# Kernel optimization log

Hardware: AMD Instinct MI355X
Metric: run time of the kernel (lower is better)

The kernel has to match this reference:

```python
import jax, jax.numpy as jnp
import numpy as np

DIM = 1024
HEADS = 16
HEAD_DIM = DIM // HEADS
SCALE = HEAD_DIM ** -0.5
HIDDEN = 4 * DIM
EPS = 1e-5


def _ln(x, g, b):
    m = jnp.mean(x, -1, keepdims=True)
    v = jnp.mean(jnp.square(x - m), -1, keepdims=True)
    return (x - m) / jnp.sqrt(v + EPS) * g + b


def _attn(x, wqkv, qb, vb, wp, bp):
    # x: (B, N, C). qkv bias = concat(q_bias, zeros, v_bias) as in the torch code.
    B, N, C = x.shape
    bias = jnp.concatenate([qb, jnp.zeros_like(vb), vb])
    qkv = (x @ wqkv.T + bias).reshape(B, N, 3, HEADS, HEAD_DIM).transpose(2, 0, 3, 1, 4)
    q, k, v = qkv[0], qkv[1], qkv[2]
    # qk_float=True: logits computed in float32
    logits = jnp.einsum('bhqd,bhkd->bhqk', (q * SCALE).astype(jnp.float32), k.astype(jnp.float32))
    a = jax.nn.softmax(logits, axis=-1).astype(x.dtype)
    o = jnp.einsum('bhqk,bhkd->bqhd', a, v).reshape(B, N, C)
    return o @ wp.T + bp


def setup_inputs() -> dict:
    key = jax.random.key(0)
    ks = jax.random.split(key, 16)
    s = 0.02
    d = {
        'x': jax.random.normal(ks[0], (4, 8, 196, DIM), jnp.float32),
        'cls_token': jax.random.normal(ks[1], (4, DIM), jnp.float32),
        # temporal branch
        'tln_g': jnp.ones((DIM,), jnp.float32), 'tln_b': jnp.zeros((DIM,), jnp.float32),
        't_wqkv': jax.random.normal(ks[2], (3 * DIM, DIM), jnp.float32) * s,
        't_qb': jax.random.normal(ks[3], (DIM,), jnp.float32) * s,
        't_vb': jax.random.normal(ks[4], (DIM,), jnp.float32) * s,
        't_wproj': jax.random.normal(ks[5], (DIM, DIM), jnp.float32) * s,
        't_bproj': jnp.zeros((DIM,), jnp.float32),
        't_fc_w': jax.random.normal(ks[6], (DIM, DIM), jnp.float32) * s,
        't_fc_b': jnp.zeros((DIM,), jnp.float32),
        # spatial branch
        'n1_g': jnp.ones((DIM,), jnp.float32), 'n1_b': jnp.zeros((DIM,), jnp.float32),
        's_wqkv': jax.random.normal(ks[7], (3 * DIM, DIM), jnp.float32) * s,
        's_qb': jax.random.normal(ks[8], (DIM,), jnp.float32) * s,
        's_vb': jax.random.normal(ks[9], (DIM,), jnp.float32) * s,
        's_wproj': jax.random.normal(ks[10], (DIM, DIM), jnp.float32) * s,
        's_bproj': jnp.zeros((DIM,), jnp.float32),
        # mlp
        'n2_g': jnp.ones((DIM,), jnp.float32), 'n2_b': jnp.zeros((DIM,), jnp.float32),
        'fc1_w': jax.random.normal(ks[11], (HIDDEN, DIM), jnp.float32) * s,
        'fc1_b': jnp.zeros((HIDDEN,), jnp.float32),
        'fc2_w': jax.random.normal(ks[12], (DIM, HIDDEN), jnp.float32) * s,
        'fc2_b': jnp.zeros((DIM,), jnp.float32),
    }
    return d


def reference(x, cls_token, tln_g, tln_b, t_wqkv, t_qb, t_vb, t_wproj, t_bproj,
              t_fc_w, t_fc_b, n1_g, n1_b, s_wqkv, s_qb, s_vb, s_wproj, s_bproj,
              n2_g, n2_b, fc1_w, fc1_b, fc2_w, fc2_b):
    B, T, N, C = x.shape
    # temporal attention: 'b t n m -> (b n) t m'
    xt = x.transpose(0, 2, 1, 3).reshape(B * N, T, C)
    xt = _attn(_ln(xt, tln_g, tln_b), t_wqkv, t_qb, t_vb, t_wproj, t_bproj)
    # '(b n) t m -> b (n t) m'
    xt = xt.reshape(B, N * T, C)
    xt = xt @ t_fc_w.T + t_fc_b
    xt = x.transpose(0, 2, 1, 3).reshape(B, N * T, C) + xt
    # spatial attention with cls token per frame
    init_cls = cls_token[:, None, :]                               # (B, 1, C)
    cls_rep = jnp.broadcast_to(init_cls, (B, T, C)).reshape(B * T, 1, C)
    xs = xt.reshape(B, N, T, C).transpose(0, 2, 1, 3).reshape(B * T, N, C)
    xs = jnp.concatenate([cls_rep, xs], axis=1)                    # (B*T, N+1, C)
    xs = _attn(_ln(xs, n1_g, n1_b), s_wqkv, s_qb, s_vb, s_wproj, s_bproj)
    cls_m = xs[:, 0, :].reshape(B, T, C).mean(axis=1, keepdims=True)  # (B, 1, C)
    xs = xs[:, 1:, :].reshape(B, T, N, C).transpose(0, 2, 1, 3).reshape(B, N * T, C)
    x2 = jnp.concatenate([init_cls, xt], axis=1) + jnp.concatenate([cls_m, xs], axis=1)
    # MLP (exact GELU, matching nn.GELU default)
    h = _ln(x2, n2_g, n2_b)
    h = jax.nn.gelu(h @ fc1_w.T + fc1_b, approximate=False) @ fc2_w.T + fc2_b
    x2 = x2 + h
    cls_out = x2[:, 0, :]
    xo = x2[:, 1:].reshape(B, N, T, C).transpose(0, 2, 1, 3)       # (B, T, N, C)
    return xo, cls_out
```

## Files before the change

### kernel.cpp

```cpp
#include <hip/hip_runtime.h>
#include <stdint.h>


#define SCALE 0.125f

typedef unsigned short u16;
typedef short bf16x8 __attribute__((ext_vector_type(8)));
typedef float f32x4 __attribute__((ext_vector_type(4)));

static constexpr int kNT    = 1568;
static constexpr int kRowsA = 6272;
static constexpr int kSeqS  = 197;
static constexpr int kRowsS = 6304;
static constexpr int kRowsC = 6276;
static constexpr size_t kXO = 6422528;

__device__ __forceinline__ float bf2f(u16 u) {
    union { unsigned int i; float f; } c; c.i = ((unsigned int)u) << 16; return c.f;
}
__device__ __forceinline__ u16 f2bf(float f) {
    union { float f; unsigned int i; } c; c.f = f;
    unsigned int r = c.i + 0x7FFFu + ((c.i >> 16) & 1u);
    return (u16)(r >> 16);
}

__device__ __forceinline__ void gll16(const void* g, void* l) {
    __builtin_amdgcn_global_load_lds((__attribute__((address_space(1))) void*)g,
                                     (__attribute__((address_space(3))) void*)l,
                                     16, 0, 0);
}

__global__ void convw_k(const float* __restrict__ in, u16* __restrict__ out, int n4) {
    const int stride = gridDim.x * blockDim.x;
    for (int i = blockIdx.x * blockDim.x + threadIdx.x; i < n4; i += stride) {
        float4 v = ((const float4*)in)[i];
        ushort4 o;
        o.x = f2bf(v.x); o.y = f2bf(v.y); o.z = f2bf(v.z); o.w = f2bf(v.w);
        ((ushort4*)out)[i] = o;
    }
}

__global__ void bias3_k(const float* __restrict__ qb, const float* __restrict__ vb,
                        float* __restrict__ dst) {
    const int i = blockIdx.x * 256 + threadIdx.x;
    if (i >= 3072) return;
    dst[i] = (i < 1024) ? qb[i] : (i < 2048) ? 0.0f : vb[i - 2048];
}

template<int MODE>
__global__ void ln_k(const float* __restrict__ src, const float* __restrict__ src2,
                     const float* __restrict__ g, const float* __restrict__ bt,
                     u16* __restrict__ out, int rows) {
    const int r = (blockIdx.x << 2) + (threadIdx.x >> 6);
    const int lane = threadIdx.x & 63;
    if (r >= rows) return;
    const float* srow;
    if constexpr (MODE == 0) {
        int b = r / kNT, rem = r - b * kNT, n = rem >> 3, t = rem & 7;
        srow = src + (((size_t)((b * 8 + t) * 196 + n)) << 10);
    } else if constexpr (MODE == 1) {
        int s2 = r / kSeqS, i = r - s2 * kSeqS, b = s2 >> 3, t = s2 & 7;
        srow = (i == 0) ? (src2 + ((size_t)b << 10))
                        : (src + (((size_t)(b * kNT + ((i - 1) << 3) + t)) << 10));
    } else {
        srow = src + ((size_t)r << 10);
    }
    float4 v[4]; float s = 0.f, ss = 0.f;
#pragma unroll
    for (int j = 0; j < 4; ++j) {
        v[j] = *(const float4*)&srow[((j << 6) + lane) << 2];
        s  += v[j].x + v[j].y + v[j].z + v[j].w;
        ss += v[j].x * v[j].x + v[j].y * v[j].y + v[j].z * v[j].z + v[j].w * v[j].w;
    }
#pragma unroll
    for (int off = 1; off < 64; off <<= 1) { s += __shfl_xor(s, off); ss += __shfl_xor(ss, off); }
    const float mean = s * (1.f / 1024.f);
    const float rstd = rsqrtf(ss * (1.f / 1024.f) - mean * mean + 1e-5f);
#pragma unroll
    for (int j = 0; j < 4; ++j) {
        const int c = ((j << 6) + lane) << 2;
        float4 gg = *(const float4*)&g[c];
        float4 bb = *(const float4*)&bt[c];
        ushort4 o;
        o.x = f2bf((v[j].x - mean) * rstd * gg.x + bb.x);
        o.y = f2bf((v[j].y - mean) * rstd * gg.y + bb.y);
        o.z = f2bf((v[j].z - mean) * rstd * gg.z + bb.z);
        o.w = f2bf((v[j].w - mean) * rstd * gg.w + bb.w);
        *(ushort4*)&out[((size_t)r << 10) + c] = o;
    }
}

template<int MODE>
__global__ void gemm_bt(const u16* __restrict__ A, const u16* __restrict__ W,
                        const float* __restrict__ bias,
                        u16* __restrict__ outB, float* __restrict__ outF,
                        const float* __restrict__ resid, float* __restrict__ dout,
                        int M, int N, int K) {
    __shared__ __align__(16) u16 As[128 * 32];
    __shared__ __align__(16) u16 Bs[128 * 32];
    const int tid  = threadIdx.x;
    const int lane = tid & 63, wave = tid >> 6;
    const int lo = lane & 15, hi = lane >> 4;
    const int wr = wave >> 1, wc = wave & 1;
    const int row0 = blockIdx.y << 7, col0 = blockIdx.x << 7;

    const int c0 = (wave << 7) + lane;
    const int c1 = c0 + 64;
    int ar0 = row0 + (c0 >> 2); if (ar0 > M - 1) ar0 = M - 1;
    int ar1 = row0 + (c1 >> 2); if (ar1 > M - 1) ar1 = M - 1;
    int br0 = col0 + (c0 >> 2); if (br0 > N - 1) br0 = N - 1;
    int br1 = col0 + (c1 >> 2); if (br1 > N - 1) br1 = N - 1;
    const u16* aS0 = A + (size_t)ar0 * K + ((c0 & 3) << 3);
    const u16* aS1 = A + (size_t)ar1 * K + ((c1 & 3) << 3);
    const u16* bS0 = W + (size_t)br0 * K + ((c0 & 3) << 3);
    const u16* bS1 = W + (size_t)br1 * K + ((c1 & 3) << 3);
    u16* lA0 = &As[wave << 10];
    u16* lA1 = &As[(wave << 10) + 512];
    u16* lB0 = &Bs[wave << 10];
    u16* lB1 = &Bs[(wave << 10) + 512];

    f32x4 acc[4][4] = {};

    for (int k0 = 0; k0 < K; k0 += 32) {
        gll16(aS0 + k0, lA0);
        gll16(aS1 + k0, lA1);
        gll16(bS0 + k0, lB0);
        gll16(bS1 + k0, lB1);
        __syncthreads();
        bf16x8 af[4], bfr[4];
#pragma unroll
        for (int m = 0; m < 4; ++m)
            af[m] = *(const bf16x8*)&As[((wr << 6) + (m << 4) + lo) * 32 + (hi << 3)];
#pragma unroll
        for (int n = 0; n < 4; ++n)
            bfr[n] = *(const bf16x8*)&Bs[((wc << 6) + (n << 4) + lo) * 32 + (hi << 3)];
#pragma unroll
        for (int m = 0; m < 4; ++m)
#pragma unroll
            for (int n = 0; n < 4; ++n)
                acc[m][n] = __builtin_amdgcn_mfma_f32_16x16x32_bf16(af[m], bfr[n], acc[m][n], 0, 0, 0);
        __syncthreads();
    }

#pragma unroll
    for (int m = 0; m < 4; ++m) {
        const int rb = row0 + (wr << 6) + (m << 4) + (hi << 2);
#pragma unroll
        for (int n = 0; n < 4; ++n) {
            const int c = col0 + (wc << 6) + (n << 4) + lo;
            const float bc = bias[c];
#pragma unroll
            for (int j = 0; j < 4; ++j) {
                const int r = rb + j;
                if (r >= M) continue;
                float v = acc[m][n][j] + bc;
                if constexpr (MODE == 2) v = 0.5f * v * (1.0f + erff(v * 0.70710678f));
                if constexpr (MODE == 3) {
                    int b = r / 1568, rem = r - b * 1568, nn = rem >> 3, tt = rem & 7;
                    v += resid[(((size_t)((b * 8 + tt) * 196 + nn)) << 10) + c];
                }
                if constexpr (MODE == 0 || MODE == 2) {
                    outB[(size_t)r * N + c] = f2bf(v);
                } else if constexpr (MODE == 1 || MODE == 3) {
                    outF[(size_t)r * N + c] = v;
                } else {
                    v += resid[((size_t)r << 10) + c];
                    int b = r / 1569, i = r - b * 1569;
                    if (i == 0) dout[kXO + ((size_t)b << 10) + c] = v;
                    else {
                        int jj = i - 1, nn = jj >> 3, tt = jj & 7;
                        dout[(((size_t)((b * 8 + tt) * 196 + nn)) << 10) + c] = v;
                    }
                }
            }
        }
    }
}

__global__ void attn_a_k(const u16* __restrict__ qkv, u16* __restrict__ o) {
    __shared__ float lq[4][8][65], lk[4][8][65], lv[4][8][65];
    __shared__ float al[4][64];
    const int lane = threadIdx.x & 63, wave = threadIdx.x >> 6;
    const int p = (blockIdx.x << 2) + wave;
    const int s = p >> 4, h = p & 15;
    const u16* base = qkv + (size_t)s * 24576 + (h << 6);
    for (int u = lane; u < 1536; u += 64) {
        const int part = u >> 9, t = (u >> 6) & 7, d = u & 63;
        const float val = bf2f(base[(size_t)t * 3072 + (part << 10) + d]);
        if (part == 0) lq[wave][t][d] = val;
        else if (part == 1) lk[wave][t][d] = val;
        else lv[wave][t][d] = val;
    }
    __syncthreads();
    const int qi = lane >> 3, kj = lane & 7;
    float dot = 0.f;
#pragma unroll
    for (int d = 0; d < 64; ++d) dot += lq[wave][qi][d] * lk[wave][kj][d];
    dot *= SCALE;
    float m = dot;
    m = fmaxf(m, __shfl_xor(m, 1));
    m = fmaxf(m, __shfl_xor(m, 2));
    m = fmaxf(m, __shfl_xor(m, 4));
    const float e = expf(dot - m);
    float sm = e;
    sm += __shfl_xor(sm, 1);
    sm += __shfl_xor(sm, 2);
    sm += __shfl_xor(sm, 4);
    al[wave][lane] = e / sm;
    __syncthreads();
    u16* orow = o + (size_t)s * 8192 + (h << 6) + lane;
#pragma unroll
    for (int ii = 0; ii < 8; ++ii) {
        float accv = 0.f;
#pragma unroll
        for (int jj = 0; jj < 8; ++jj) accv += al[wave][(ii << 3) + jj] * lv[wave][jj][lane];
        orow[(size_t)ii * 1024] = f2bf(accv);
    }
}

__global__ __launch_bounds__(256, 2) void attn_s_mfma(const u16* __restrict__ qkv,
                                                      u16* __restrict__ o) {
    __shared__ __align__(16) u16 SM[29696];
    u16* __restrict__ Vt = SM;
    const int tid = threadIdx.x, lane = tid & 63, wave = tid >> 6;
    const int lo = lane & 15, hi = lane >> 4;
    u16* __restrict__ Pw = SM + 14848 + wave * 3712;
    const int s2 = blockIdx.x >> 4, h = blockIdx.x & 15;
    const u16* __restrict__ base = qkv + (size_t)s2 * (kSeqS * 3072) + (h << 6);

    for (int u = tid; u < 26 * 64; u += 256) {
        const int d = u & 63, k0 = (u >> 6) << 3;
        union { bf16x8 v; u16 e[8]; } pk;
#pragma unroll
        for (int i = 0; i < 8; ++i) {
            int kr = k0 + i; if (kr > 196) kr = 196;
            pk.e[i] = base[(size_t)kr * 3072 + 2048 + d];
        }
        *(bf16x8*)&Vt[d * 232 + k0] = pk.v;
    }
    for (int u = tid; u < 1024; u += 256)
        Vt[(u >> 4) * 232 + 208 + (u & 15)] = 0;
    for (int u = lane; u < 256; u += 64)
        Pw[(u >> 4) * 232 + 208 + (u & 15)] = 0;
    __syncthreads();

    for (int qt = wave; qt < 13; qt += 4) {
        int qr = qt * 16 + lo; if (qr > 196) qr = 196;
        const u16* qp = base + (size_t)qr * 3072;
        const bf16x8 aq0 = *(const bf16x8*)&qp[hi << 3];
        const bf16x8 aq1 = *(const bf16x8*)&qp[32 + (hi << 3)];

        f32x4 s[13];
#pragma unroll
        for (int kt = 0; kt < 13; ++kt) {
            int kr = kt * 16 + lo; if (kr > 196) kr = 196;
            const u16* kp = base + (size_t)kr * 3072 + 1024;
            const bf16x8 bk0 = *(const bf16x8*)&kp[hi << 3];
            const bf16x8 bk1 = *(const bf16x8*)&kp[32 + (hi << 3)];
            f32x4 acc = {};
            acc = __builtin_amdgcn_mfma_f32_16x16x32_bf16(aq0, bk0, acc, 0, 0, 0);
            acc = __builtin_amdgcn_mfma_f32_16x16x32_bf16(aq1, bk1, acc, 0, 0, 0);
            s[kt] = acc * SCALE;
        }
        if (lo > 4) s[12] = (f32x4){-1e30f, -1e30f, -1e30f, -1e30f};

        float inv[4];
#pragma unroll
        for (int j = 0; j < 4; ++j) {
            float m = s[0][j];
#pragma unroll
            for (int kt = 1; kt < 13; ++kt) m = fmaxf(m, s[kt][j]);
            m = fmaxf(m, __shfl_xor(m, 1));
            m = fmaxf(m, __shfl_xor(m, 2));
            m = fmaxf(m, __shfl_xor(m, 4));
            m = fmaxf(m, __shfl_xor(m, 8));
            float sum = 0.f;
#pragma unroll
            for (int kt = 0; kt < 13; ++kt) {
                const float e = __expf(s[kt][j] - m);
                s[kt][j] = e;
                sum += e;
            }
            sum += __shfl_xor(sum, 1);
            sum += __shfl_xor(sum, 2);
            sum += __shfl_xor(sum, 4);
            sum += __shfl_xor(sum, 8);
            inv[j] = 1.f / sum;
        }

#pragma unroll
        for (int kt = 0; kt < 13; ++kt)
#pragma unroll
            for (int j = 0; j < 4; ++j)
                Pw[((hi << 2) + j) * 232 + kt * 16 + lo] = f2bf(s[kt][j]);

        f32x4 o4[4] = {};
#pragma unroll
        for (int kc = 0; kc < 7; ++kc) {
            const bf16x8 pa = *(const bf16x8*)&Pw[lo * 232 + kc * 32 + (hi << 3)];
#pragma unroll
            for (int dt = 0; dt < 4; ++dt) {
                const bf16x8 vf = *(const bf16x8*)&Vt[(dt * 16 + lo) * 232 + kc * 32 + (hi << 3)];
                o4[dt] = __builtin_amdgcn_mfma_f32_16x16x32_bf16(pa, vf, o4[dt], 0, 0, 0);
            }
        }

#pragma unroll
        for (int j = 0; j < 4; ++j) {
            const int q = qt * 16 + (hi << 2) + j;
            if (q > 196) continue;
            u16* orow = o + (((size_t)(s2 * kSeqS + q)) << 10) + (h << 6);
#pragma unroll
            for (int dt = 0; dt < 4; ++dt)
                orow[dt * 16 + lo] = f2bf(o4[dt][j] * inv[j]);
        }
    }
}

__global__ void clsm_k(const float* __restrict__ xs, float* __restrict__ cm) {
    const int idx = blockIdx.x * 256 + threadIdx.x;
    if (idx >= 4096) return;
    const int b = idx >> 10, c = idx & 1023;
    float s = 0.f;
#pragma unroll
    for (int t = 0; t < 8; ++t) s += xs[(((size_t)(b * 8 + t)) * kSeqS) * 1024 + c];
    cm[idx] = s * 0.125f;
}

__global__ void build_x2_k(const float* __restrict__ xt, const float* __restrict__ xs,
                           const float* __restrict__ cls, const float* __restrict__ cm,
                           float* __restrict__ x2) {
    const int r = blockIdx.x;
    const int c = threadIdx.x << 2;
    const int b = r / 1569, i = r - b * 1569;
    const float* pa; const float* pb;
    if (i == 0) {
        pa = cls + ((size_t)b << 10) + c;
        pb = cm + ((size_t)b << 10) + c;
    } else {
        const int jj = i - 1, n = jj >> 3, t = jj & 7;
        pa = xt + (((size_t)(b * 1568 + jj)) << 10) + c;
        pb = xs + (((size_t)((b * 8 + t) * kSeqS + 1 + n)) << 10) + c;
    }
    const float4 va = *(const float4*)pa;
    const float4 vb = *(const float4*)pb;
    float4 vo;
    vo.x = va.x + vb.x; vo.y = va.y + vb.y; vo.z = va.z + vb.z; vo.w = va.w + vb.w;
    *(float4*)&x2[((size_t)r << 10) + c] = vo;
}

extern "C" void kernel_launch(void* const* d_in, const int* in_sizes, int n_in,
                              void* d_out, int out_size, void* d_ws, size_t ws_size,
                              hipStream_t stream) {
    const float* x       = (const float*)d_in[0];
    const float* cls     = (const float*)d_in[1];
    const float* tln_g   = (const float*)d_in[2];
    const float* tln_b   = (const float*)d_in[3];
    const float* t_wqkv  = (const float*)d_in[4];
    const float* t_qb    = (const float*)d_in[5];
    const float* t_vb    = (const float*)d_in[6];
    const float* t_wproj = (const float*)d_in[7];
    const float* t_bproj = (const float*)d_in[8];
    const float* t_fc_w  = (const float*)d_in[9];
    const float* t_fc_b  = (const float*)d_in[10];
    const float* n1_g    = (const float*)d_in[11];
    const float* n1_b    = (const float*)d_in[12];
    const float* s_wqkv  = (const float*)d_in[13];
    const float* s_qb    = (const float*)d_in[14];
    const float* s_vb    = (const float*)d_in[15];
    const float* s_wproj = (const float*)d_in[16];
    const float* s_bproj = (const float*)d_in[17];
    const float* n2_g    = (const float*)d_in[18];
    const float* n2_b    = (const float*)d_in[19];
    const float* fc1_w   = (const float*)d_in[20];
    const float* fc1_b   = (const float*)d_in[21];
    const float* fc2_w   = (const float*)d_in[22];
    const float* fc2_b   = (const float*)d_in[23];
    float* dout = (float*)d_out;
    char* ws = (char*)d_ws;

    size_t off = 0;
    auto alloc = [&](size_t bytes) { size_t o = off; off += (bytes + 255) & ~(size_t)255; return o; };

    u16* t_wqkv_bf  = (u16*)(ws + alloc(3145728ull * 2));
    u16* t_wproj_bf = (u16*)(ws + alloc(1048576ull * 2));
    u16* t_fcw_bf   = (u16*)(ws + alloc(1048576ull * 2));
    u16* s_wqkv_bf  = (u16*)(ws + alloc(3145728ull * 2));
    u16* s_wproj_bf = (u16*)(ws + alloc(1048576ull * 2));
    u16* fc1_bf     = (u16*)(ws + alloc(4194304ull * 2));
    u16* fc2_bf     = (u16*)(ws + alloc(4194304ull * 2));
    u16* ln_bf      = (u16*)(ws + alloc((size_t)kRowsS * 1024 * 2));
    u16* qkv_bf     = (u16*)(ws + alloc((size_t)kRowsS * 3072 * 2));
    u16* o_bf       = (u16*)(ws + alloc((size_t)kRowsS * 1024 * 2));
    u16* h1_bf      = qkv_bf;
    u16* mid_bf     = (u16*)(ws + alloc((size_t)kRowsA * 1024 * 2));
    float* xt_f     = (float*)(ws + alloc((size_t)kRowsA * 1024 * 4));
    float* xs_f     = (float*)(ws + alloc((size_t)kRowsS * 1024 * 4));
    float* x2_f     = (float*)(ws + alloc((size_t)kRowsC * 1024 * 4));
    float* bias_t   = (float*)(ws + alloc(3072 * 4));
    float* bias_s   = (float*)(ws + alloc(3072 * 4));
    float* clsm     = (float*)(ws + alloc(4096 * 4));
    (void)ws_size; (void)in_sizes; (void)n_in; (void)out_size;

    convw_k<<<dim3(1024), dim3(256), 0, stream>>>(t_wqkv, t_wqkv_bf, 786432);
    convw_k<<<dim3(512),  dim3(256), 0, stream>>>(t_wproj, t_wproj_bf, 262144);
    convw_k<<<dim3(512),  dim3(256), 0, stream>>>(t_fc_w, t_fcw_bf, 262144);
    convw_k<<<dim3(1024), dim3(256), 0, stream>>>(s_wqkv, s_wqkv_bf, 786432);
    convw_k<<<dim3(512),  dim3(256), 0, stream>>>(s_wproj, s_wproj_bf, 262144);
    convw_k<<<dim3(1024), dim3(256), 0, stream>>>(fc1_w, fc1_bf, 1048576);
    convw_k<<<dim3(1024), dim3(256), 0, stream>>>(fc2_w, fc2_bf, 1048576);
    bias3_k<<<dim3(12), dim3(256), 0, stream>>>(t_qb, t_vb, bias_t);
    bias3_k<<<dim3(12), dim3(256), 0, stream>>>(s_qb, s_vb, bias_s);

    ln_k<0><<<dim3(kRowsA / 4), dim3(256), 0, stream>>>(x, nullptr, tln_g, tln_b, ln_bf, kRowsA);
    gemm_bt<0><<<dim3(24, 49), dim3(256), 0, stream>>>(ln_bf, t_wqkv_bf, bias_t, qkv_bf, nullptr, nullptr, nullptr, kRowsA, 3072, 1024);
    attn_a_k<<<dim3(3136), dim3(256), 0, stream>>>(qkv_bf, o_bf);
    gemm_bt<0><<<dim3(8, 49), dim3(256), 0, stream>>>(o_bf, t_wproj_bf, t_bproj, mid_bf, nullptr, nullptr, nullptr, kRowsA, 1024, 1024);
    gemm_bt<3><<<dim3(8, 49), dim3(256), 0, stream>>>(mid_bf, t_fcw_bf, t_fc_b, nullptr, xt_f, x, nullptr, kRowsA, 1024, 1024);

    ln_k<1><<<dim3(kRowsS / 4), dim3(256), 0, stream>>>(xt_f, cls, n1_g, n1_b, ln_bf, kRowsS);
    gemm_bt<0><<<dim3(24, 50), dim3(256), 0, stream>>>(ln_bf, s_wqkv_bf, bias_s, qkv_bf, nullptr, nullptr, nullptr, kRowsS, 3072, 1024);
    attn_s_mfma<<<dim3(512), dim3(256), 0, stream>>>(qkv_bf, o_bf);
    gemm_bt<1><<<dim3(8, 50), dim3(256), 0, stream>>>(o_bf, s_wproj_bf, s_bproj, nullptr, xs_f, nullptr, nullptr, kRowsS, 1024, 1024);
    clsm_k<<<dim3(16), dim3(256), 0, stream>>>(xs_f, clsm);
    build_x2_k<<<dim3(kRowsC), dim3(256), 0, stream>>>(xt_f, xs_f, cls, clsm, x2_f);

    ln_k<2><<<dim3(kRowsC / 4), dim3(256), 0, stream>>>(x2_f, nullptr, n2_g, n2_b, ln_bf, kRowsC);
    gemm_bt<2><<<dim3(32, 50), dim3(256), 0, stream>>>(ln_bf, fc1_bf, fc1_b, h1_bf, nullptr, nullptr, nullptr, kRowsC, 4096, 1024);
    gemm_bt<4><<<dim3(8, 50), dim3(256), 0, stream>>>(h1_bf, fc2_bf, fc2_b, nullptr, nullptr, x2_f, dout, kRowsC, 1024, 4096);
}
```

Baseline: 550.9 us.

## Double-buffer GEMM LDS tiles with K=64 steps and XOR-swizzled layout

```diff
diff --git a/kernel.cpp b/kernel.cpp
--- a/kernel.cpp
+++ b/kernel.cpp
@@ -91,55 +91,83 @@
 }
 
 template<int MODE>
-__global__ void gemm_bt(const u16* __restrict__ A, const u16* __restrict__ W,
-                        const float* __restrict__ bias,
-                        u16* __restrict__ outB, float* __restrict__ outF,
-                        const float* __restrict__ resid, float* __restrict__ dout,
-                        int M, int N, int K) {
-    __shared__ __align__(16) u16 As[128 * 32];
-    __shared__ __align__(16) u16 Bs[128 * 32];
+__global__ __launch_bounds__(256, 2) void gemm_bt(
+        const u16* __restrict__ A, const u16* __restrict__ W,
+        const float* __restrict__ bias,
+        u16* __restrict__ outB, float* __restrict__ outF,
+        const float* __restrict__ resid, float* __restrict__ dout,
+        int M, int N, int K) {
+    __shared__ __align__(16) u16 As[2][8192];
+    __shared__ __align__(16) u16 Bs[2][8192];
     const int tid  = threadIdx.x;
     const int lane = tid & 63, wave = tid >> 6;
     const int lo = lane & 15, hi = lane >> 4;
     const int wr = wave >> 1, wc = wave & 1;
     const int row0 = blockIdx.y << 7, col0 = blockIdx.x << 7;
 
-    const int c0 = (wave << 7) + lane;
-    const int c1 = c0 + 64;
-    int ar0 = row0 + (c0 >> 2); if (ar0 > M - 1) ar0 = M - 1;
-    int ar1 = row0 + (c1 >> 2); if (ar1 > M - 1) ar1 = M - 1;
-    int br0 = col0 + (c0 >> 2); if (br0 > N - 1) br0 = N - 1;
-    int br1 = col0 + (c1 >> 2); if (br1 > N - 1) br1 = N - 1;
-    const u16* aS0 = A + (size_t)ar0 * K + ((c0 & 3) << 3);
-    const u16* aS1 = A + (size_t)ar1 * K + ((c1 & 3) << 3);
-    const u16* bS0 = W + (size_t)br0 * K + ((c0 & 3) << 3);
-    const u16* bS1 = W + (size_t)br1 * K + ((c1 & 3) << 3);
-    u16* lA0 = &As[wave << 10];
-    u16* lA1 = &As[(wave << 10) + 512];
-    u16* lB0 = &Bs[wave << 10];
-    u16* lB1 = &Bs[(wave << 10) + 512];
+    const u16* aP[4]; const u16* bP[4];
+#pragma unroll
+    for (int i = 0; i < 4; ++i) {
+        const int c = (wave << 8) + (i << 6) + lane;
+        const int row = c >> 3;
+        const int jl = ((c & 7) ^ (row & 7)) << 3;
+        int ar = row0 + row; if (ar > M - 1) ar = M - 1;
+        int br = col0 + row; if (br > N - 1) br = N - 1;
+        aP[i] = A + (size_t)ar * K + jl;
+        bP[i] = W + (size_t)br * K + jl;
+    }
 
     f32x4 acc[4][4] = {};
-
-    for (int k0 = 0; k0 < K; k0 += 32) {
-        gll16(aS0 + k0, lA0);
-        gll16(aS1 + k0, lA1);
-        gll16(bS0 + k0, lB0);
-        gll16(bS1 + k0, lB1);
-        __syncthreads();
-        bf16x8 af[4], bfr[4];
+    const int nk = K >> 6;
+
+#pragma unroll
+    for (int i = 0; i < 4; ++i) {
+        u16* dA = &As[0][(wave << 11) + (i << 9)];
+        u16* dB = &Bs[0][(wave << 11) + (i << 9)];
+        gll16(aP[i], dA);
+        gll16(bP[i], dB);
+    }
+    __syncthreads();
+
+    int cur = 0;
+    for (int it = 0; it < nk; ++it) {
+        const bool more = (it + 1) < nk;
+        if (more) {
+            const int k1 = (it + 1) << 6;
+#pragma unroll
+            for (int i = 0; i < 4; ++i) {
+                u16* dA = &As[cur ^ 1][(wave << 11) + (i << 9)];
+                u16* dB = &Bs[cur ^ 1][(wave << 11) + (i << 9)];
+                gll16(aP[i] + k1, dA);
+                gll16(bP[i] + k1, dB);
+            }
+        }
+        bf16x8 af[4][2], bfr[4][2];
+#pragma unroll
+        for (int m = 0; m < 4; ++m) {
+            const int row = (wr << 6) + (m << 4) + lo;
+#pragma unroll
+            for (int h = 0; h < 2; ++h)
+                af[m][h] = *(const bf16x8*)&As[cur][(row << 6) + ((((h << 2) + hi) ^ (lo & 7)) << 3)];
+        }
+#pragma unroll
+        for (int n = 0; n < 4; ++n) {
+            const int row = (wc << 6) + (n << 4) + lo;
+#pragma unroll
+            for (int h = 0; h < 2; ++h)
+                bfr[n][h] = *(const bf16x8*)&Bs[cur][(row << 6) + ((((h << 2) + hi) ^ (lo & 7)) << 3)];
+        }
 #pragma unroll
         for (int m = 0; m < 4; ++m)
-            af[m] = *(const bf16x8*)&As[((wr << 6) + (m << 4) + lo) * 32 + (hi << 3)];
-#pragma unroll
-        for (int n = 0; n < 4; ++n)
-            bfr[n] = *(const bf16x8*)&Bs[((wc << 6) + (n << 4) + lo) * 32 + (hi << 3)];
-#pragma unroll
-        for (int m = 0; m < 4; ++m)
-#pragma unroll
-            for (int n = 0; n < 4; ++n)
-                acc[m][n] = __builtin_amdgcn_mfma_f32_16x16x32_bf16(af[m], bfr[n], acc[m][n], 0, 0, 0);
-        __syncthreads();
+#pragma unroll
+            for (int n = 0; n < 4; ++n) {
+                acc[m][n] = __builtin_amdgcn_mfma_f32_16x16x32_bf16(af[m][0], bfr[n][0], acc[m][n], 0, 0, 0);
+                acc[m][n] = __builtin_amdgcn_mfma_f32_16x16x32_bf16(af[m][1], bfr[n][1], acc[m][n], 0, 0, 0);
+            }
+        if (more) {
+            __syncthreads();
+            cur ^= 1;
+        }
     }
 
 #pragma unroll
```

Result: no change. 554.8 us (+0.7%).
